# Kernel optimization log

Measured on AMD Instinct MI355X. Metric: run time of the kernel, lower is better.

Reference implementation:

```python
import jax, jax.numpy as jnp
import numpy as np

THRESHOLD = 15.0
INIT_RATIO = 0.5
WINDOW_T = 100
C1 = INIT_RATIO * THRESHOLD            # 7.5, initial membrane potential
C2 = 1.0 / THRESHOLD                   # 1/15
C3 = (1.0 - INIT_RATIO) / WINDOW_T     # 0.005


def snn_layer(spikes, mem, hat_spikes, W, b):
    """One SNNLinear layer in training mode.
    spikes: [T,B,in], mem: [B,out], hat_spikes: [B,in], W: [out,in], b: [out].
    Returns (ss [T,B,out], mem_final [B,out], hat_s [B,out]).
    """
    T = spikes.shape[0]
    # delta_us = fc(spikes): [T,B,out]
    delta_us = jnp.einsum('tbi,oi->tbo', spikes, W) + b

    def step(carry, du):
        m, sum_u = carry
        m = m + du
        s = (m > THRESHOLD).astype(m.dtype)
        m = jnp.clip(m, 0.0, THRESHOLD)
        sum_u = sum_u + m
        m = m - m * s  # reset to 0 where spiked
        return (m, sum_u), s

    (mem_f, sum_u), ss = jax.lax.scan(step, (mem, jnp.zeros_like(mem)), delta_us)
    # In torch this loop runs under no_grad
    ss = jax.lax.stop_gradient(ss)
    mem_f = jax.lax.stop_gradient(mem_f)
    hat_s_fwd = jnp.mean(ss, axis=0)
    hat_u_fwd = jax.lax.stop_gradient(sum_u) / T

    # delta_u = fc(hat_spikes): grad path
    delta_u = hat_spikes @ W.T + b
    # ForwardFirstBackwardSecond: forward value hat_u_fwd, gradient flows to delta_u
    hat_u = hat_u_fwd + (delta_u - jax.lax.stop_gradient(delta_u))
    g = jnp.maximum(hat_u * C2, C3)
    hat_s = hat_s_fwd + (g - jax.lax.stop_gradient(g))
    return ss, mem_f, hat_s


def setup_inputs() -> dict:
    key = jax.random.key(0)
    ks = jax.random.split(key, 8)
    T, B = 50, 256
    shapes = [1024, 2048, 2048, 1024]
    spikes = jax.random.bernoulli(ks[0], 0.1, (T, B, shapes[0])).astype(jnp.float32)
    hat_spk = jax.random.uniform(ks[1], (B, shapes[0]), jnp.float32) * 0.2
    mem0 = jnp.full((B, shapes[1]), C1, jnp.float32)
    mem1 = jnp.full((B, shapes[2]), C1, jnp.float32)
    mem2 = jnp.full((B, shapes[3]), C1, jnp.float32)
    W0 = jax.random.normal(ks[2], (shapes[1], shapes[0]), jnp.float32)
    b0 = jax.random.normal(ks[3], (shapes[1],), jnp.float32)
    W1 = jax.random.normal(ks[4], (shapes[2], shapes[1]), jnp.float32)
    b1 = jax.random.normal(ks[5], (shapes[2],), jnp.float32)
    W2 = jax.random.normal(ks[6], (shapes[3], shapes[2]), jnp.float32)
    b2 = jax.random.normal(ks[7], (shapes[3],), jnp.float32)
    return {"spikes": spikes, "hat_spk": hat_spk, "mem0": mem0, "mem1": mem1,
            "mem2": mem2, "W0": W0, "b0": b0, "W1": W1, "b1": b1, "W2": W2, "b2": b2}


def reference(spikes, hat_spk, mem0, mem1, mem2, W0, b0, W1, b1, W2, b2):
    s, _, h = snn_layer(spikes, mem0, hat_spk, W0, b0)
    s, _, h = snn_layer(s, mem1, h, W1, b1)
    s, _, h = snn_layer(s, mem2, h, W2, b2)
    return s, h
```

## Files before the change

### kernel.cpp

```cpp
#include <hip/hip_runtime.h>
#include <cstdint>
#include <cstddef>

#define T_STEPS 50
#define BATCH   256
#define TC      10

__global__ __launch_bounds__(256)
void pack_spikes_k(const float* __restrict__ A, uint32_t* __restrict__ P) {
    const int i    = (int)blockIdx.x * 256 + (int)threadIdx.x;
    const int lane = (int)threadIdx.x & 63;
    const unsigned long long m = __ballot(A[i] != 0.0f);
    if ((lane & 31) == 0)
        P[i >> 5] = (uint32_t)((lane & 32) ? (m >> 32) : m);
}


template<int K, int O>
__global__ __launch_bounds__(256)
void gemm_k(const uint32_t* __restrict__ Ain,
            const float* __restrict__ W,
            const float* __restrict__ bias,
            float* __restrict__ DU)
{
    constexpr int NW = K / 32;
    __shared__ float Wsm[2][32][256];

    const int tid = (int)threadIdx.x;
    const int o_l = tid & 63;
    const int wid = tid >> 6;
    const int o0  = (int)blockIdx.x * 256;
    const int oq  = o0 + 4 * o_l;
    const int b_u = __builtin_amdgcn_readfirstlane((int)blockIdx.y * 4 + wid);
    const int tc0 = (int)blockIdx.z * TC;
    const uint32_t* __restrict__ Ab = Ain + (size_t)b_u * NW;

    const float4 bb4 = *(const float4*)(bias + oq);

    float pre[TC][4], cur[TC][4];
#pragma unroll
    for (int tt = 0; tt < TC; ++tt)
#pragma unroll
        for (int c = 0; c < 4; ++c) { pre[tt][c] = 0.0f; cur[tt][c] = 0.0f; }

    const int s_i    = tid;
    const int s_orow0 = s_i >> 3;
    const int s_q    = s_i & 7;

    float4 pf[8];
#pragma unroll
    for (int r = 0; r < 8; ++r)
        pf[r] = *(const float4*)(W + (size_t)(o0 + s_orow0 + r * 32) * K + s_q * 4);
    uint32_t Mc[TC], Mn[TC];
#pragma unroll
    for (int tt = 0; tt < TC; ++tt)
        Mc[tt] = __builtin_amdgcn_readfirstlane(
                     Ab[(size_t)(tc0 + tt) * (BATCH * NW) + 0]);
#pragma unroll
    for (int r = 0; r < 8; ++r) {
        const int orow = s_orow0 + r * 32;
        const int pc   = (((orow >> 2) ^ s_q) << 2) | (orow & 3);
        Wsm[0][4 * s_q + 0][pc] = pf[r].x;
        Wsm[0][4 * s_q + 1][pc] = pf[r].y;
        Wsm[0][4 * s_q + 2][pc] = pf[r].z;
        Wsm[0][4 * s_q + 3][pc] = pf[r].w;
    }
    __syncthreads();

    for (int wt = 0; wt < NW; ++wt) {
        const int cb = wt & 1;
        if (wt + 1 < NW) {
#pragma unroll
            for (int r = 0; r < 8; ++r)
                pf[r] = *(const float4*)(W + (size_t)(o0 + s_orow0 + r * 32) * K
                                           + (wt + 1) * 32 + s_q * 4);
#pragma unroll
            for (int tt = 0; tt < TC; ++tt)
                Mn[tt] = __builtin_amdgcn_readfirstlane(
                             Ab[(size_t)(tc0 + tt) * (BATCH * NW) + (wt + 1)]);
        }

#pragma unroll 8
        for (int kk = 0; kk < 32; ++kk) {
            const float4 wv = *(const float4*)&Wsm[cb][kk][(o_l ^ ((kk >> 2) & 7)) << 2];
#pragma unroll
            for (int tt = 0; tt < TC; ++tt) {
                const uint32_t fb = ((Mc[tt] >> kk) & 1u) ? 0x3f800000u : 0u;
                const float f = __builtin_bit_cast(float, fb);
                cur[tt][0] = __builtin_fmaf(f, wv.x, cur[tt][0]);
                cur[tt][1] = __builtin_fmaf(f, wv.y, cur[tt][1]);
                cur[tt][2] = __builtin_fmaf(f, wv.z, cur[tt][2]);
                cur[tt][3] = __builtin_fmaf(f, wv.w, cur[tt][3]);
            }
        }

        if (wt + 1 < NW) {
#pragma unroll
            for (int r = 0; r < 8; ++r) {
                const int orow = s_orow0 + r * 32;
                const int pc   = (((orow >> 2) ^ s_q) << 2) | (orow & 3);
                Wsm[cb ^ 1][4 * s_q + 0][pc] = pf[r].x;
                Wsm[cb ^ 1][4 * s_q + 1][pc] = pf[r].y;
                Wsm[cb ^ 1][4 * s_q + 2][pc] = pf[r].z;
                Wsm[cb ^ 1][4 * s_q + 3][pc] = pf[r].w;
            }
        }
        __syncthreads();

#pragma unroll
        for (int tt = 0; tt < TC; ++tt)
            Mc[tt] = Mn[tt];

        if (((wt + 1) & 15) == 0) {
#pragma unroll
            for (int tt = 0; tt < TC; ++tt)
#pragma unroll
                for (int c = 0; c < 4; ++c) {
                    pre[tt][c] = pre[tt][c] + cur[tt][c];
                    cur[tt][c] = 0.0f;
                }
        }
    }

#pragma unroll
    for (int tt = 0; tt < TC; ++tt) {
        const int t = tc0 + tt;
        float4 du;
        du.x = (pre[tt][0] + cur[tt][0]) + bb4.x;
        du.y = (pre[tt][1] + cur[tt][1]) + bb4.y;
        du.z = (pre[tt][2] + cur[tt][2]) + bb4.z;
        du.w = (pre[tt][3] + cur[tt][3]) + bb4.w;
        *(float4*)(DU + (size_t)t * (BATCH * O) + (size_t)b_u * O + oq) = du;
    }
}

template<int O, bool LAST>
__global__ __launch_bounds__(256)
void scan_k(const float* __restrict__ DU,
            const float* __restrict__ mem,
            uint32_t* __restrict__ Pout,
            float* __restrict__ SSout,
            float* __restrict__ Hout)
{
    constexpr int NWO = O / 32;
    __shared__ unsigned char pk[4][64];

    const int tid = (int)threadIdx.x;
    const int o_l = tid & 63;
    const int wid = tid >> 6;
    const int b   = (int)blockIdx.y;
    const int o0  = (int)blockIdx.x * 1024 + wid * 256;
    const int oq  = o0 + 4 * o_l;

    float4 m4 = *(const float4*)(mem + (size_t)b * O + oq);
    int c0 = 0, c1 = 0, c2 = 0, c3 = 0;

    float4 du = *(const float4*)(DU + (size_t)b * O + oq);

    for (int t = 0; t < T_STEPS; ++t) {
        float4 dun;
        if (t + 1 < T_STEPS)
            dun = *(const float4*)(DU + (size_t)(t + 1) * (BATCH * O) + (size_t)b * O + oq);
        m4.x += du.x; m4.y += du.y; m4.z += du.z; m4.w += du.w;
        const bool s0 = m4.x > 15.0f, s1 = m4.y > 15.0f,
                   s2 = m4.z > 15.0f, s3 = m4.w > 15.0f;
        m4.x = fminf(fmaxf(m4.x, 0.0f), 15.0f);
        m4.y = fminf(fmaxf(m4.y, 0.0f), 15.0f);
        m4.z = fminf(fmaxf(m4.z, 0.0f), 15.0f);
        m4.w = fminf(fmaxf(m4.w, 0.0f), 15.0f);
        if (s0) { m4.x = 0.0f; ++c0; }
        if (s1) { m4.y = 0.0f; ++c1; }
        if (s2) { m4.z = 0.0f; ++c2; }
        if (s3) { m4.w = 0.0f; ++c3; }

        if (LAST) {
            *(float4*)(SSout + (size_t)t * (BATCH * O) + (size_t)b * O + oq) =
                make_float4(s0 ? 1.0f : 0.0f, s1 ? 1.0f : 0.0f,
                            s2 ? 1.0f : 0.0f, s3 ? 1.0f : 0.0f);
        } else {
            pk[wid][o_l] = (unsigned char)((s0 ? 1 : 0) | (s1 ? 2 : 0) |
                                           (s2 ? 4 : 0) | (s3 ? 8 : 0));
            __syncthreads();
            if (o_l < 8) {
                const uint2 d = *(const uint2*)&pk[wid][o_l * 8];
                uint32_t x = d.x & 0x0F0F0F0Fu;
                x = (x | (x >> 4)) & 0x00FF00FFu;
                x = (x | (x >> 8)) & 0x0000FFFFu;
                uint32_t y = d.y & 0x0F0F0F0Fu;
                y = (y | (y >> 4)) & 0x00FF00FFu;
                y = (y | (y >> 8)) & 0x0000FFFFu;
                Pout[(size_t)t * (BATCH * NWO) + (size_t)b * NWO + (o0 >> 5) + o_l]
                    = x | (y << 16);
            }
            __syncthreads();
        }
        du = dun;
    }
    if (LAST) {
        *(float4*)(Hout + (size_t)b * O + oq) =
            make_float4((float)c0 / 50.0f, (float)c1 / 50.0f,
                        (float)c2 / 50.0f, (float)c3 / 50.0f);
    }
}

template<int K, int O, bool LAST>
__global__ __launch_bounds__(256)
void snn_k(const uint32_t* __restrict__ Ain,
           const float* __restrict__ W,
           const float* __restrict__ bias,
           const float* __restrict__ mem,
           uint32_t* __restrict__ Pout,
           float* __restrict__ SSout,
           float* __restrict__ Hout)
{
    constexpr int NW  = K / 32;
    constexpr int NWO = O / 32;
    __shared__ float Wsm[32][256];
    __shared__ unsigned char pk[4][64];

    const int tid = (int)threadIdx.x;
    const int o_l = tid & 63;
    const int wid = tid >> 6;
    const int o0  = (int)blockIdx.x * 256;
    const int oq  = o0 + 4 * o_l;
    const int b_u = __builtin_amdgcn_readfirstlane((int)blockIdx.y * 4 + wid);
    const uint32_t* __restrict__ Ab = Ain + (size_t)b_u * NW;

    float4 m4 = *(const float4*)(mem + (size_t)b_u * O + oq);
    const float4 bb4 = *(const float4*)(bias + oq);
    int c0 = 0, c1 = 0, c2 = 0, c3 = 0;

    for (int tc0 = 0; tc0 < T_STEPS; tc0 += TC) {
        float pre[TC][4], cur[TC][4];
#pragma unroll
        for (int tt = 0; tt < TC; ++tt)
#pragma unroll
            for (int c = 0; c < 4; ++c) { pre[tt][c] = 0.0f; cur[tt][c] = 0.0f; }

        for (int wt = 0; wt < NW; ++wt) {
#pragma unroll
            for (int r = 0; r < 8; ++r) {
                const int i    = tid + r * 256;
                const int orow = i >> 3;
                const int q    = i & 7;
                const float4 v = *(const float4*)(W + (size_t)(o0 + orow) * K + wt * 32 + q * 4);
                const int pc   = (((orow >> 2) ^ q) << 2) | (orow & 3);
                Wsm[4 * q + 0][pc] = v.x;
                Wsm[4 * q + 1][pc] = v.y;
                Wsm[4 * q + 2][pc] = v.z;
                Wsm[4 * q + 3][pc] = v.w;
            }
            uint32_t M[TC];
#pragma unroll
            for (int tt = 0; tt < TC; ++tt)
                M[tt] = Ab[(size_t)(tc0 + tt) * (BATCH * NW) + wt];
            __syncthreads();

#pragma unroll 8
            for (int kk = 0; kk < 32; ++kk) {
                const float4 wv = *(const float4*)&Wsm[kk][(o_l ^ ((kk >> 2) & 7)) << 2];
#pragma unroll
                for (int tt = 0; tt < TC; ++tt) {
                    const float f = __builtin_bit_cast(float, ((M[tt] >> kk) & 1u) * 0x3f800000u);
                    cur[tt][0] = __builtin_fmaf(f, wv.x, cur[tt][0]);
                    cur[tt][1] = __builtin_fmaf(f, wv.y, cur[tt][1]);
                    cur[tt][2] = __builtin_fmaf(f, wv.z, cur[tt][2]);
                    cur[tt][3] = __builtin_fmaf(f, wv.w, cur[tt][3]);
                }
            }
            __syncthreads();

            if (((wt + 1) & 15) == 0) {
#pragma unroll
                for (int tt = 0; tt < TC; ++tt)
#pragma unroll
                    for (int c = 0; c < 4; ++c) {
                        pre[tt][c] = pre[tt][c] + cur[tt][c];
                        cur[tt][c] = 0.0f;
                    }
            }
        }

#pragma unroll
        for (int tt = 0; tt < TC; ++tt) {
            const int t = tc0 + tt;
            const float du0 = (pre[tt][0] + cur[tt][0]) + bb4.x;
            const float du1 = (pre[tt][1] + cur[tt][1]) + bb4.y;
            const float du2 = (pre[tt][2] + cur[tt][2]) + bb4.z;
            const float du3 = (pre[tt][3] + cur[tt][3]) + bb4.w;
            m4.x += du0; m4.y += du1; m4.z += du2; m4.w += du3;
            const bool s0 = m4.x > 15.0f, s1 = m4.y > 15.0f,
                       s2 = m4.z > 15.0f, s3 = m4.w > 15.0f;
            m4.x = fminf(fmaxf(m4.x, 0.0f), 15.0f);
            m4.y = fminf(fmaxf(m4.y, 0.0f), 15.0f);
            m4.z = fminf(fmaxf(m4.z, 0.0f), 15.0f);
            m4.w = fminf(fmaxf(m4.w, 0.0f), 15.0f);
            if (s0) { m4.x = 0.0f; ++c0; }
            if (s1) { m4.y = 0.0f; ++c1; }
            if (s2) { m4.z = 0.0f; ++c2; }
            if (s3) { m4.w = 0.0f; ++c3; }

            if (LAST) {
                *(float4*)(SSout + (size_t)t * (BATCH * O) + (size_t)b_u * O + oq) =
                    make_float4(s0 ? 1.0f : 0.0f, s1 ? 1.0f : 0.0f,
                                s2 ? 1.0f : 0.0f, s3 ? 1.0f : 0.0f);
            } else {
                pk[wid][o_l] = (unsigned char)((s0 ? 1 : 0) | (s1 ? 2 : 0) |
                                               (s2 ? 4 : 0) | (s3 ? 8 : 0));
                __syncthreads();
                if (o_l < 8) {
                    const uint2 d = *(const uint2*)&pk[wid][o_l * 8];
                    uint32_t x = d.x & 0x0F0F0F0Fu;
                    x = (x | (x >> 4)) & 0x00FF00FFu;
                    x = (x | (x >> 8)) & 0x0000FFFFu;
                    uint32_t y = d.y & 0x0F0F0F0Fu;
                    y = (y | (y >> 4)) & 0x00FF00FFu;
                    y = (y | (y >> 8)) & 0x0000FFFFu;
                    Pout[(size_t)t * (BATCH * NWO) + (size_t)b_u * NWO + (o0 >> 5) + o_l]
                        = x | (y << 16);
                }
                __syncthreads();
            }
        }
    }
    if (LAST) {
        *(float4*)(Hout + (size_t)b_u * O + oq) =
            make_float4((float)c0 / 50.0f, (float)c1 / 50.0f,
                        (float)c2 / 50.0f, (float)c3 / 50.0f);
    }
}

extern "C" void kernel_launch(void* const* d_in, const int* in_sizes, int n_in,
                              void* d_out, int out_size, void* d_ws, size_t ws_size,
                              hipStream_t stream) {
    (void)out_size;

    const float *spikes = nullptr, *mem0 = nullptr, *mem1 = nullptr, *mem2 = nullptr;
    const float *W0 = nullptr, *b0 = nullptr, *W1 = nullptr, *b1 = nullptr;
    const float *W2 = nullptr, *b2 = nullptr;
    int n2048 = 0, nW02 = 0, nMem = 0, n262k = 0;
    for (int i = 0; i < n_in; ++i) {
        const float* p = (const float*)d_in[i];
        switch (in_sizes[i]) {
            case 13107200: spikes = p; break;
            case 4194304:  W1 = p; break;
            case 1024:     b2 = p; break;
            case 2097152:  if (nW02++ == 0) W0 = p; else W2 = p; break;
            case 2048:     if (n2048++ == 0) b0 = p; else b1 = p; break;
            case 524288:   if (nMem++ == 0) mem0 = p; else mem1 = p; break;
            case 262144:   if (n262k++ == 0) ; else mem2 = p; break;
            default: break;
        }
    }
    if (!spikes || !W0 || !W1 || !W2 || !b0 || !b1 || !b2 || !mem0 || !mem1 || !mem2) {
        spikes = (const float*)d_in[0];
        mem0 = (const float*)d_in[2]; mem1 = (const float*)d_in[3];
        mem2 = (const float*)d_in[4];
        W0 = (const float*)d_in[5]; b0 = (const float*)d_in[6];
        W1 = (const float*)d_in[7]; b1 = (const float*)d_in[8];
        W2 = (const float*)d_in[9]; b2 = (const float*)d_in[10];
    }

    uint32_t* P0 = (uint32_t*)d_ws;
    uint32_t* P1 = (uint32_t*)((char*)d_ws + (2u << 20));
    uint32_t* P2 = (uint32_t*)((char*)d_ws + (6u << 20));
    float*    DU = (float*)((char*)d_ws + (16u << 20));

    float* out_s = (float*)d_out;
    float* out_h = out_s + (size_t)T_STEPS * BATCH * 1024;

    const int n_sp = T_STEPS * BATCH * 1024;
    pack_spikes_k<<<n_sp / 256, 256, 0, stream>>>(spikes, P0);

    const size_t need = (size_t)(16u << 20)
                      + (size_t)T_STEPS * BATCH * 2048 * sizeof(float);

    if (ws_size >= need) {
        gemm_k<1024, 2048><<<dim3(8, 64, 5), dim3(256), 0, stream>>>(P0, W0, b0, DU);
        scan_k<2048, false><<<dim3(2, BATCH), dim3(256), 0, stream>>>(
            DU, mem0, P1, nullptr, nullptr);
        gemm_k<2048, 2048><<<dim3(8, 64, 5), dim3(256), 0, stream>>>(P1, W1, b1, DU);
        scan_k<2048, false><<<dim3(2, BATCH), dim3(256), 0, stream>>>(
            DU, mem1, P2, nullptr, nullptr);
        gemm_k<2048, 1024><<<dim3(4, 64, 5), dim3(256), 0, stream>>>(P2, W2, b2, DU);
        scan_k<1024, true><<<dim3(1, BATCH), dim3(256), 0, stream>>>(
            DU, mem2, nullptr, out_s, out_h);
    } else {
        snn_k<1024, 2048, false><<<dim3(8, 64), dim3(256), 0, stream>>>(
            P0, W0, b0, mem0, P1, nullptr, nullptr);
        snn_k<2048, 2048, false><<<dim3(8, 64), dim3(256), 0, stream>>>(
            P1, W1, b1, mem1, P2, nullptr, nullptr);
        snn_k<2048, 1024, true><<<dim3(4, 64), dim3(256), 0, stream>>>(
            P2, W2, b2, mem2, nullptr, out_s, out_h);
    }
}
```

Measured before the change: 3.426 ms.

## Triple-buffer weight tiles in 16-wide K chunks with single barrier per chunk

Restructures the GEMM weight staging from a double-buffered 32-wide K tile to a triple-buffered 16-wide K chunk. The global prefetch now runs two chunks ahead and the LDS write happens one chunk ahead, with a single barrier per chunk. The goal is to hide global-load latency better and cut the per-thread prefetch register footprint from 8 to 4 float4s. The cost is twice as many barriers, plus extra bookkeeping to split the 32-bit spike masks across half-chunks.

```diff
diff --git a/kernel.cpp b/kernel.cpp
--- a/kernel.cpp
+++ b/kernel.cpp
@@ -23,8 +23,9 @@
             const float* __restrict__ bias,
             float* __restrict__ DU)
 {
-    constexpr int NW = K / 32;
-    __shared__ float Wsm[2][32][256];
+    constexpr int NW  = K / 32;
+    constexpr int NCH = K / 16;
+    __shared__ float Wsm[3][16][256];
 
     const int tid = (int)threadIdx.x;
     const int o_l = tid & 63;
@@ -37,55 +38,81 @@
 
     const float4 bb4 = *(const float4*)(bias + oq);
 
+    const int s_orow0 = tid >> 2;
+    const int s_q4    = tid & 3;
+
     float pre[TC][4], cur[TC][4];
 #pragma unroll
     for (int tt = 0; tt < TC; ++tt)
 #pragma unroll
         for (int c = 0; c < 4; ++c) { pre[tt][c] = 0.0f; cur[tt][c] = 0.0f; }
 
-    const int s_i    = tid;
-    const int s_orow0 = s_i >> 3;
-    const int s_q    = s_i & 7;
-
-    float4 pf[8];
-#pragma unroll
-    for (int r = 0; r < 8; ++r)
-        pf[r] = *(const float4*)(W + (size_t)(o0 + s_orow0 + r * 32) * K + s_q * 4);
+    float4 pf[4];
+#pragma unroll
+    for (int r = 0; r < 4; ++r)
+        pf[r] = *(const float4*)(W + (size_t)(o0 + s_orow0 + r * 64) * K + s_q4 * 4);
+#pragma unroll
+    for (int r = 0; r < 4; ++r) {
+        const int orow = s_orow0 + r * 64;
+        const int pc   = ((((orow >> 2) ^ (s_q4 << 1)) << 2) | (orow & 3));
+        Wsm[0][4 * s_q4 + 0][pc] = pf[r].x;
+        Wsm[0][4 * s_q4 + 1][pc] = pf[r].y;
+        Wsm[0][4 * s_q4 + 2][pc] = pf[r].z;
+        Wsm[0][4 * s_q4 + 3][pc] = pf[r].w;
+    }
+#pragma unroll
+    for (int r = 0; r < 4; ++r)
+        pf[r] = *(const float4*)(W + (size_t)(o0 + s_orow0 + r * 64) * K + 16 + s_q4 * 4);
     uint32_t Mc[TC], Mn[TC];
 #pragma unroll
-    for (int tt = 0; tt < TC; ++tt)
+    for (int tt = 0; tt < TC; ++tt) {
         Mc[tt] = __builtin_amdgcn_readfirstlane(
                      Ab[(size_t)(tc0 + tt) * (BATCH * NW) + 0]);
-#pragma unroll
-    for (int r = 0; r < 8; ++r) {
-        const int orow = s_orow0 + r * 32;
-        const int pc   = (((orow >> 2) ^ s_q) << 2) | (orow & 3);
-        Wsm[0][4 * s_q + 0][pc] = pf[r].x;
-        Wsm[0][4 * s_q + 1][pc] = pf[r].y;
-        Wsm[0][4 * s_q + 2][pc] = pf[r].z;
-        Wsm[0][4 * s_q + 3][pc] = pf[r].w;
-    }
-    __syncthreads();
-
-    for (int wt = 0; wt < NW; ++wt) {
-        const int cb = wt & 1;
-        if (wt + 1 < NW) {
-#pragma unroll
-            for (int r = 0; r < 8; ++r)
-                pf[r] = *(const float4*)(W + (size_t)(o0 + s_orow0 + r * 32) * K
-                                           + (wt + 1) * 32 + s_q * 4);
+        Mn[tt] = 0u;
+    }
+
+    for (int c = 0; c < NCH; ++c) {
+        if (c + 1 < NCH) {
+#pragma unroll
+            for (int r = 0; r < 4; ++r) {
+                const int orow = s_orow0 + r * 64;
+                const int pc   = ((((orow >> 2) ^ (s_q4 << 1)) << 2) | (orow & 3));
+                float* dst = &Wsm[(c + 1) % 3][0][0];
+                dst[(4 * s_q4 + 0) * 256 + pc] = pf[r].x;
+                dst[(4 * s_q4 + 1) * 256 + pc] = pf[r].y;
+                dst[(4 * s_q4 + 2) * 256 + pc] = pf[r].z;
+                dst[(4 * s_q4 + 3) * 256 + pc] = pf[r].w;
+            }
+        }
+        if (c + 2 < NCH) {
+#pragma unroll
+            for (int r = 0; r < 4; ++r)
+                pf[r] = *(const float4*)(W + (size_t)(o0 + s_orow0 + r * 64) * K
+                                           + (c + 2) * 16 + s_q4 * 4);
+        }
+        if ((c & 1) == 0 && (c >> 1) + 1 < NW) {
 #pragma unroll
             for (int tt = 0; tt < TC; ++tt)
                 Mn[tt] = __builtin_amdgcn_readfirstlane(
-                             Ab[(size_t)(tc0 + tt) * (BATCH * NW) + (wt + 1)]);
-        }
-
-#pragma unroll 8
-        for (int kk = 0; kk < 32; ++kk) {
-            const float4 wv = *(const float4*)&Wsm[cb][kk][(o_l ^ ((kk >> 2) & 7)) << 2];
+                             Ab[(size_t)(tc0 + tt) * (BATCH * NW) + (c >> 1) + 1]);
+        }
+        asm volatile("s_waitcnt lgkmcnt(0)" ::: "memory");
+        __builtin_amdgcn_s_barrier();
+        asm volatile("" ::: "memory");
+
+        const float* src = &Wsm[c % 3][0][0];
+        uint32_t Mh[TC];
+        const int bo = (c & 1) << 4;
+#pragma unroll
+        for (int tt = 0; tt < TC; ++tt)
+            Mh[tt] = Mc[tt] >> bo;
+#pragma unroll
+        for (int kk = 0; kk < 16; ++kk) {
+            const float4 wv = *(const float4*)&src[kk * 256 +
+                                  ((o_l ^ ((kk >> 2) << 1)) << 2)];
 #pragma unroll
             for (int tt = 0; tt < TC; ++tt) {
-                const uint32_t fb = ((Mc[tt] >> kk) & 1u) ? 0x3f800000u : 0u;
+                const uint32_t fb = ((Mh[tt] >> kk) & 1u) ? 0x3f800000u : 0u;
                 const float f = __builtin_bit_cast(float, fb);
                 cur[tt][0] = __builtin_fmaf(f, wv.x, cur[tt][0]);
                 cur[tt][1] = __builtin_fmaf(f, wv.y, cur[tt][1]);
@@ -94,30 +121,18 @@
             }
         }
 
-        if (wt + 1 < NW) {
-#pragma unroll
-            for (int r = 0; r < 8; ++r) {
-                const int orow = s_orow0 + r * 32;
-                const int pc   = (((orow >> 2) ^ s_q) << 2) | (orow & 3);
-                Wsm[cb ^ 1][4 * s_q + 0][pc] = pf[r].x;
-                Wsm[cb ^ 1][4 * s_q + 1][pc] = pf[r].y;
-                Wsm[cb ^ 1][4 * s_q + 2][pc] = pf[r].z;
-                Wsm[cb ^ 1][4 * s_q + 3][pc] = pf[r].w;
-            }
-        }
-        __syncthreads();
-
-#pragma unroll
-        for (int tt = 0; tt < TC; ++tt)
-            Mc[tt] = Mn[tt];
-
-        if (((wt + 1) & 15) == 0) {
+        if (c & 1) {
 #pragma unroll
             for (int tt = 0; tt < TC; ++tt)
-#pragma unroll
-                for (int c = 0; c < 4; ++c) {
-                    pre[tt][c] = pre[tt][c] + cur[tt][c];
-                    cur[tt][c] = 0.0f;
+                Mc[tt] = Mn[tt];
+        }
+        if (((c + 1) & 31) == 0) {
+#pragma unroll
+            for (int tt = 0; tt < TC; ++tt)
+#pragma unroll
+                for (int cc = 0; cc < 4; ++cc) {
+                    pre[tt][cc] = pre[tt][cc] + cur[tt][cc];
+                    cur[tt][cc] = 0.0f;
                 }
         }
     }
```

Result: faster. 2.977 ms (-13.1%).
